# Optimization experiments

Measured on AMD Instinct MI355X. Metric: run time of the kernel, lower is better.

The kernel has to match this reference:

```python
import jax, jax.numpy as jnp
import numpy as np

D_MODEL, H, D_K, D_V = 512, 8, 64, 64
S_Q, S_KV = 2048, 2048


def setup_inputs() -> dict:
    key = jax.random.key(0)
    ks = jax.random.split(key, 11)
    sc = 0.02
    return {
        "embeddings": jax.random.normal(ks[0], (S_Q, D_MODEL), jnp.float32),
        "K": jax.random.normal(ks[1], (S_KV, D_MODEL), jnp.float32),
        "V": jax.random.normal(ks[2], (S_KV, D_MODEL), jnp.float32),
        # per-head projection weights (stacked over heads) + biases
        "Wq": jax.random.normal(ks[3], (H, D_MODEL, D_K), jnp.float32) * sc,
        "bq": jax.random.normal(ks[4], (H, D_K), jnp.float32) * sc,
        "Wk": jax.random.normal(ks[5], (H, D_MODEL, D_K), jnp.float32) * sc,
        "bk": jax.random.normal(ks[6], (H, D_K), jnp.float32) * sc,
        "Wv": jax.random.normal(ks[7], (H, D_MODEL, D_V), jnp.float32) * sc,
        "bv": jax.random.normal(ks[8], (H, D_V), jnp.float32) * sc,
        # final linear: [h*d_v -> d_model]
        "Wo": jax.random.normal(ks[9], (H * D_V, D_MODEL), jnp.float32) * sc,
        "bo": jax.random.normal(ks[10], (D_MODEL,), jnp.float32) * sc,
    }


def reference(embeddings, K, V, Wq, bq, Wk, bk, Wv, bv, Wo, bo):
    # Batched per-head projections (the original loops over h heads; math identical)
    q = jnp.einsum("sd,hdk->hsk", embeddings, Wq) + bq[:, None, :]  # [h, Sq, d_k]
    k = jnp.einsum("td,hdk->htk", K, Wk) + bk[:, None, :]           # [h, Skv, d_k]
    v = jnp.einsum("td,hdv->htv", V, Wv) + bv[:, None, :]           # [h, Skv, d_v]
    scores = jnp.einsum("hsk,htk->hst", q, k) / jnp.sqrt(jnp.asarray(D_K, q.dtype))
    attn = jax.nn.softmax(scores, axis=-1)                           # [h, Sq, Skv]
    out = jnp.einsum("hst,htv->hsv", attn, v)                        # [h, Sq, d_v]
    # torch.cat(results, dim=1): head 0's d_v columns first -> [Sq, h*d_v]
    concat = jnp.transpose(out, (1, 0, 2)).reshape(S_Q, H * D_V)
    return concat @ Wo + bo                                          # [Sq, d_model]
```

## Files before the change

### kernel.cpp

```cpp
#include <hip/hip_runtime.h>

#define SQ 2048
#define DM 512
#define NH 8
#define NSPLIT 4

typedef __bf16 bf16x8 __attribute__((ext_vector_type(8)));
typedef float f32x4 __attribute__((ext_vector_type(4)));
typedef unsigned short us8 __attribute__((ext_vector_type(8)));

__device__ __forceinline__ unsigned short f2bf(float f) {
    unsigned u = __builtin_bit_cast(unsigned, f);
    u += 0x7fffu + ((u >> 16) & 1u);
    return (unsigned short)(u >> 16);
}
__device__ __forceinline__ unsigned short f2bf_trunc(float f) {
    return (unsigned short)(__builtin_bit_cast(unsigned, f) >> 16);
}

__global__ __launch_bounds__(256) void convert_all(
    const float* __restrict__ emb, const float* __restrict__ Kin, const float* __restrict__ Vin,
    const float* __restrict__ Wq,  const float* __restrict__ Wk,  const float* __restrict__ Wv,
    const float* __restrict__ Wo,
    unsigned short* __restrict__ xe, unsigned short* __restrict__ xk, unsigned short* __restrict__ xv,
    unsigned short* __restrict__ Wt, unsigned short* __restrict__ Wot)
{
    const int b = blockIdx.x, tid = threadIdx.x;
    __shared__ float ld[64 * 68];
    float4* ld4 = reinterpret_cast<float4*>(ld);

    if (b < 1536) {
        const int m = b >> 9;
        const float* src = (m == 0) ? emb : (m == 1) ? Kin : Vin;
        unsigned short* dst = (m == 0) ? xe : (m == 1) ? xk : xv;
        const int oct = (b & 511) * 256 + tid;
        const float4* s4 = reinterpret_cast<const float4*>(src + (size_t)oct * 8);
        float4 f0 = s4[0], f1 = s4[1];
        us8 o;
        o[0] = f2bf(f0.x); o[1] = f2bf(f0.y); o[2] = f2bf(f0.z); o[3] = f2bf(f0.w);
        o[4] = f2bf(f1.x); o[5] = f2bf(f1.y); o[6] = f2bf(f1.z); o[7] = f2bf(f1.w);
        *reinterpret_cast<us8*>(dst + (size_t)oct * 8) = o;
    } else if (b < 1728) {
        const int wi = b - 1536;
        const int idx = wi >> 3;
        const int kt = wi & 7;
        const int p = idx >> 3, h = idx & 7;
        const float* src = ((p == 0) ? Wq : (p == 1) ? Wk : Wv)
                         + (size_t)h * 512 * 64 + (size_t)kt * 64 * 64;
        unsigned short* dst = Wt + (size_t)idx * 64 * 512 + kt * 64;
        const int rr = tid >> 4, c4 = tid & 15;
        #pragma unroll
        for (int it = 0; it < 4; it++) {
            int r = rr + 16 * it;
            ld4[r * 17 + c4] = reinterpret_cast<const float4*>(src + (size_t)r * 64)[c4];
        }
        __syncthreads();
        #pragma unroll
        for (int it = 0; it < 2; it++) {
            int slot = tid + it * 256;
            int n = slot >> 3, g = slot & 7;
            us8 o;
            #pragma unroll
            for (int i = 0; i < 8; i++)
                o[i] = f2bf(ld[(g * 8 + i) * 68 + n]);
            *reinterpret_cast<us8*>(dst + (size_t)n * 512 + g * 8) = o;
        }
    } else {
        const int ti = b - 1728;
        const int kt = ti >> 3, nt = ti & 7;
        const float* src = Wo + (size_t)kt * 64 * 512 + nt * 64;
        const int rr = tid >> 4, c4 = tid & 15;
        #pragma unroll
        for (int it = 0; it < 4; it++) {
            int r = rr + 16 * it;
            ld4[r * 17 + c4] = reinterpret_cast<const float4*>(src + (size_t)r * 512)[c4];
        }
        __syncthreads();
        #pragma unroll
        for (int it = 0; it < 2; it++) {
            int slot = tid + it * 256;
            int n = slot >> 3, g = slot & 7;
            us8 o;
            #pragma unroll
            for (int i = 0; i < 8; i++)
                o[i] = f2bf(ld[(g * 8 + i) * 68 + n]);
            *reinterpret_cast<us8*>(Wot + (size_t)(nt * 64 + n) * 512 + kt * 64 + g * 8) = o;
        }
    }
}

__global__ __launch_bounds__(256) void qkv_mfma(
    const unsigned short* __restrict__ xe, const unsigned short* __restrict__ xk,
    const unsigned short* __restrict__ xv, const unsigned short* __restrict__ Wt,
    const float* __restrict__ bq, const float* __restrict__ bk, const float* __restrict__ bv,
    unsigned short* __restrict__ qo, unsigned short* __restrict__ ko, unsigned short* __restrict__ vo)
{
    const int p = blockIdx.z, h = blockIdx.y, s0 = blockIdx.x * 64;
    const unsigned short* X = (p == 0) ? xe : (p == 1) ? xk : xv;
    const unsigned short* W = Wt + (size_t)(p * 8 + h) * 64 * 512;
    const float* B = ((p == 0) ? bq : (p == 1) ? bk : bv) + h * 64;

    const int tid = threadIdx.x;
    const int w = tid >> 6, lane = tid & 63, cl = lane & 15, q4 = lane >> 4;
    const int sr = tid >> 3, sg = tid & 7;

    __shared__ unsigned short As[2][64 * 72];
    __shared__ unsigned short Bs[2][64 * 72];

    #pragma unroll
    for (int it = 0; it < 2; it++) {
        int r = sr + 32 * it;
        *reinterpret_cast<float4*>(&As[0][r * 72 + sg * 8]) =
            *reinterpret_cast<const float4*>(&X[(size_t)(s0 + r) * 512 + sg * 8]);
        *reinterpret_cast<float4*>(&Bs[0][r * 72 + sg * 8]) =
            *reinterpret_cast<const float4*>(&W[(size_t)r * 512 + sg * 8]);
    }

    f32x4 acc[4] = {};

    for (int c = 0; c < 8; c++) {
        __syncthreads();
        const int buf = c & 1;
        const bool more = (c + 1 < 8);
        float4 ar[2], br[2];
        if (more) {
            #pragma unroll
            for (int it = 0; it < 2; it++) {
                int r = sr + 32 * it;
                ar[it] = *reinterpret_cast<const float4*>(
                    &X[(size_t)(s0 + r) * 512 + (c + 1) * 64 + sg * 8]);
                br[it] = *reinterpret_cast<const float4*>(
                    &W[(size_t)r * 512 + (c + 1) * 64 + sg * 8]);
            }
        }

        bf16x8 a0 = *reinterpret_cast<const bf16x8*>(&As[buf][(16 * w + cl) * 72 + q4 * 8]);
        bf16x8 a1 = *reinterpret_cast<const bf16x8*>(&As[buf][(16 * w + cl) * 72 + 32 + q4 * 8]);
        #pragma unroll
        for (int nn = 0; nn < 4; nn++) {
            bf16x8 b0 = *reinterpret_cast<const bf16x8*>(&Bs[buf][(16 * nn + cl) * 72 + q4 * 8]);
            bf16x8 b1 = *reinterpret_cast<const bf16x8*>(&Bs[buf][(16 * nn + cl) * 72 + 32 + q4 * 8]);
            acc[nn] = __builtin_amdgcn_mfma_f32_16x16x32_bf16(a0, b0, acc[nn], 0, 0, 0);
            acc[nn] = __builtin_amdgcn_mfma_f32_16x16x32_bf16(a1, b1, acc[nn], 0, 0, 0);
        }

        if (more) {
            const int nbuf = buf ^ 1;
            #pragma unroll
            for (int it = 0; it < 2; it++) {
                int r = sr + 32 * it;
                *reinterpret_cast<float4*>(&As[nbuf][r * 72 + sg * 8]) = ar[it];
                *reinterpret_cast<float4*>(&Bs[nbuf][r * 72 + sg * 8]) = br[it];
            }
        }
    }

    if (p == 0) {
        #pragma unroll
        for (int nn = 0; nn < 4; nn++) {
            int col = 16 * nn + cl;
            float bb = B[col];
            #pragma unroll
            for (int r = 0; r < 4; r++)
                qo[((size_t)h * SQ + s0 + 16 * w + q4 * 4 + r) * 64 + col] =
                    f2bf((acc[nn][r] + bb) * 0.125f);
        }
    } else if (p == 1) {
        #pragma unroll
        for (int nn = 0; nn < 4; nn++) {
            int col = 16 * nn + cl;
            float bb = B[col];
            #pragma unroll
            for (int r = 0; r < 4; r++)
                ko[((size_t)h * SQ + s0 + 16 * w + q4 * 4 + r) * 64 + col] =
                    f2bf(acc[nn][r] + bb);
        }
    } else {
        #pragma unroll
        for (int nn = 0; nn < 4; nn++) {
            int col = 16 * nn + cl;
            float bb = B[col];
            ushort4 o;
            o.x = f2bf(acc[nn][0] + bb);
            o.y = f2bf(acc[nn][1] + bb);
            o.z = f2bf(acc[nn][2] + bb);
            o.w = f2bf(acc[nn][3] + bb);
            *reinterpret_cast<ushort4*>(
                vo + ((size_t)h * 64 + col) * SQ + s0 + 16 * w + q4 * 4) = o;
        }
    }
}

#define PW 72

__global__ __launch_bounds__(256) void attn_fwd(
    const unsigned short* __restrict__ qbf,
    const unsigned short* __restrict__ kbf,
    const unsigned short* __restrict__ vbf,
    float* __restrict__ Opart,
    float* __restrict__ lpart)
{
    const int h = blockIdx.y, s0 = blockIdx.x * 64, z = blockIdx.z;
    const int tid = threadIdx.x;
    const int w = tid >> 6, lane = tid & 63, cl = lane & 15, q4 = lane >> 4;
    const int NT = SQ / 64 / NSPLIT;
    const int t0 = z * NT;

    __shared__ unsigned short Ks[2][64 * PW];
    __shared__ unsigned short Vs[2][64 * PW];
    __shared__ unsigned short Ps[4][16 * PW];

    bf16x8 aq0 = *reinterpret_cast<const bf16x8*>(
        &qbf[((size_t)h * SQ + s0 + 16 * w + cl) * 64 + q4 * 8]);
    bf16x8 aq1 = *reinterpret_cast<const bf16x8*>(
        &qbf[((size_t)h * SQ + s0 + 16 * w + cl) * 64 + 32 + q4 * 8]);

    const int sr = tid >> 3, sg = tid & 7;

    #pragma unroll
    for (int it = 0; it < 2; it++) {
        int r = sr + 32 * it;
        *reinterpret_cast<float4*>(&Ks[0][r * PW + sg * 8]) =
            *reinterpret_cast<const float4*>(&kbf[((size_t)h * SQ + t0 * 64 + r) * 64 + sg * 8]);
        *reinterpret_cast<float4*>(&Vs[0][r * PW + sg * 8]) =
            *reinterpret_cast<const float4*>(&vbf[((size_t)h * 64 + r) * SQ + t0 * 64 + sg * 8]);
    }

    f32x4 o_acc[4] = {};
    float lsum[4] = {};

    for (int tl = 0; tl < NT; tl++) {
        __syncthreads();
        const int buf = tl & 1;
        const bool more = (tl + 1 < NT);
        float4 kr[2], vr[2];
        if (more) {
            #pragma unroll
            for (int it = 0; it < 2; it++) {
                int r = sr + 32 * it;
                kr[it] = *reinterpret_cast<const float4*>(
                    &kbf[((size_t)h * SQ + (t0 + tl + 1) * 64 + r) * 64 + sg * 8]);
                vr[it] = *reinterpret_cast<const float4*>(
                    &vbf[((size_t)h * 64 + r) * SQ + (t0 + tl + 1) * 64 + sg * 8]);
            }
        }

        f32x4 s_acc[4] = {};
        #pragma unroll
        for (int nn = 0; nn < 4; nn++) {
            bf16x8 b0 = *reinterpret_cast<const bf16x8*>(&Ks[buf][(16 * nn + cl) * PW + q4 * 8]);
            bf16x8 b1 = *reinterpret_cast<const bf16x8*>(&Ks[buf][(16 * nn + cl) * PW + 32 + q4 * 8]);
            s_acc[nn] = __builtin_amdgcn_mfma_f32_16x16x32_bf16(aq0, b0, s_acc[nn], 0, 0, 0);
            s_acc[nn] = __builtin_amdgcn_mfma_f32_16x16x32_bf16(aq1, b1, s_acc[nn], 0, 0, 0);
        }

        #pragma unroll
        for (int r = 0; r < 4; r++) {
            #pragma unroll
            for (int nn = 0; nn < 4; nn++) {
                float pv = __expf(s_acc[nn][r]);
                lsum[r] += pv;
                Ps[w][(q4 * 4 + r) * PW + 16 * nn + cl] = f2bf_trunc(pv);
            }
        }
        bf16x8 ap0 = *reinterpret_cast<const bf16x8*>(&Ps[w][cl * PW + q4 * 8]);
        bf16x8 ap1 = *reinterpret_cast<const bf16x8*>(&Ps[w][cl * PW + 32 + q4 * 8]);

        #pragma unroll
        for (int nn = 0; nn < 4; nn++) {
            bf16x8 b0 = *reinterpret_cast<const bf16x8*>(&Vs[buf][(16 * nn + cl) * PW + q4 * 8]);
            bf16x8 b1 = *reinterpret_cast<const bf16x8*>(&Vs[buf][(16 * nn + cl) * PW + 32 + q4 * 8]);
            o_acc[nn] = __builtin_amdgcn_mfma_f32_16x16x32_bf16(ap0, b0, o_acc[nn], 0, 0, 0);
            o_acc[nn] = __builtin_amdgcn_mfma_f32_16x16x32_bf16(ap1, b1, o_acc[nn], 0, 0, 0);
        }

        if (more) {
            const int nbuf = buf ^ 1;
            #pragma unroll
            for (int it = 0; it < 2; it++) {
                int r = sr + 32 * it;
                *reinterpret_cast<float4*>(&Ks[nbuf][r * PW + sg * 8]) = kr[it];
                *reinterpret_cast<float4*>(&Vs[nbuf][r * PW + sg * 8]) = vr[it];
            }
        }
    }

    #pragma unroll
    for (int r = 0; r < 4; r++) {
        float v = lsum[r];
        #pragma unroll
        for (int off = 1; off < 16; off <<= 1) v += __shfl_xor(v, off);
        lsum[r] = v;
    }

    const size_t zb = (size_t)(z * NH + h);
    if (cl == 0) {
        #pragma unroll
        for (int r = 0; r < 4; r++)
            lpart[zb * SQ + s0 + 16 * w + q4 * 4 + r] = lsum[r];
    }
    #pragma unroll
    for (int nn = 0; nn < 4; nn++)
        #pragma unroll
        for (int r = 0; r < 4; r++)
            Opart[(zb * SQ + s0 + 16 * w + q4 * 4 + r) * 64 + 16 * nn + cl] = o_acc[nn][r];
}

__global__ __launch_bounds__(256) void out_proj(
    const float* __restrict__ Opart, const float* __restrict__ lpart,
    const unsigned short* __restrict__ Wot,
    const float* __restrict__ bo, float* __restrict__ out)
{
    const int s0 = blockIdx.x * 64, n0 = blockIdx.y * 64;
    const int tid = threadIdx.x;
    const int w = tid >> 6, lane = tid & 63, cl = lane & 15, q4 = lane >> 4;
    const int sr = tid >> 3, sg = tid & 7;

    __shared__ unsigned short As[2][64 * 72];
    __shared__ unsigned short Bs[2][64 * 72];
    __shared__ float invL[512];

    #pragma unroll
    for (int k = 0; k < 2; k++) {
        int idx = tid * 2 + k;
        int hh = idx >> 6, ss = idx & 63;
        float l = 0.f;
        #pragma unroll
        for (int z = 0; z < NSPLIT; z++)
            l += lpart[(size_t)(z * 8 + hh) * SQ + s0 + ss];
        invL[idx] = 1.0f / l;
    }
    __syncthreads();

    #pragma unroll
    for (int it = 0; it < 2; it++) {
        int r = sr + 32 * it;
        float o[8] = {};
        #pragma unroll
        for (int z = 0; z < NSPLIT; z++) {
            const float4* pp = reinterpret_cast<const float4*>(
                &Opart[((size_t)(z * 8) * SQ + s0 + r) * 64 + sg * 8]);
            float4 a = pp[0], b = pp[1];
            o[0] += a.x; o[1] += a.y; o[2] += a.z; o[3] += a.w;
            o[4] += b.x; o[5] += b.y; o[6] += b.z; o[7] += b.w;
        }
        float il = invL[r];
        us8 pk;
        #pragma unroll
        for (int i = 0; i < 8; i++) pk[i] = f2bf(o[i] * il);
        *reinterpret_cast<us8*>(&As[0][r * 72 + sg * 8]) = pk;
        *reinterpret_cast<float4*>(&Bs[0][r * 72 + sg * 8]) =
            *reinterpret_cast<const float4*>(&Wot[(size_t)(n0 + r) * 512 + sg * 8]);
    }

    f32x4 acc[4] = {};

    for (int c = 0; c < 8; c++) {
        __syncthreads();
        const int buf = c & 1;
        const bool more = (c + 1 < 8);
        float4 pre[2][NSPLIT][2];
        float4 wr[2];
        if (more) {
            const int hn = c + 1;
            #pragma unroll
            for (int it = 0; it < 2; it++) {
                int r = sr + 32 * it;
                #pragma unroll
                for (int z = 0; z < NSPLIT; z++) {
                    const float4* pp = reinterpret_cast<const float4*>(
                        &Opart[((size_t)(z * 8 + hn) * SQ + s0 + r) * 64 + sg * 8]);
                    pre[it][z][0] = pp[0];
                    pre[it][z][1] = pp[1];
                }
                wr[it] = *reinterpret_cast<const float4*>(
                    &Wot[(size_t)(n0 + r) * 512 + hn * 64 + sg * 8]);
            }
        }

        bf16x8 a0 = *reinterpret_cast<const bf16x8*>(&As[buf][(16 * w + cl) * 72 + q4 * 8]);
        bf16x8 a1 = *reinterpret_cast<const bf16x8*>(&As[buf][(16 * w + cl) * 72 + 32 + q4 * 8]);
        #pragma unroll
        for (int nn = 0; nn < 4; nn++) {
            bf16x8 b0 = *reinterpret_cast<const bf16x8*>(&Bs[buf][(16 * nn + cl) * 72 + q4 * 8]);
            bf16x8 b1 = *reinterpret_cast<const bf16x8*>(&Bs[buf][(16 * nn + cl) * 72 + 32 + q4 * 8]);
            acc[nn] = __builtin_amdgcn_mfma_f32_16x16x32_bf16(a0, b0, acc[nn], 0, 0, 0);
            acc[nn] = __builtin_amdgcn_mfma_f32_16x16x32_bf16(a1, b1, acc[nn], 0, 0, 0);
        }

        if (more) {
            const int nbuf = buf ^ 1;
            const int hn = c + 1;
            #pragma unroll
            for (int it = 0; it < 2; it++) {
                int r = sr + 32 * it;
                float o[8] = {};
                #pragma unroll
                for (int z = 0; z < NSPLIT; z++) {
                    float4 a = pre[it][z][0], b = pre[it][z][1];
                    o[0] += a.x; o[1] += a.y; o[2] += a.z; o[3] += a.w;
                    o[4] += b.x; o[5] += b.y; o[6] += b.z; o[7] += b.w;
                }
                float il = invL[hn * 64 + r];
                us8 pk;
                #pragma unroll
                for (int i = 0; i < 8; i++) pk[i] = f2bf(o[i] * il);
                *reinterpret_cast<us8*>(&As[nbuf][r * 72 + sg * 8]) = pk;
                *reinterpret_cast<float4*>(&Bs[nbuf][r * 72 + sg * 8]) = wr[it];
            }
        }
    }

    #pragma unroll
    for (int nn = 0; nn < 4; nn++) {
        int col = n0 + 16 * nn + cl;
        float bb = bo[col];
        #pragma unroll
        for (int r = 0; r < 4; r++)
            out[(size_t)(s0 + 16 * w + q4 * 4 + r) * DM + col] = acc[nn][r] + bb;
    }
}

extern "C" void kernel_launch(void* const* d_in, const int* in_sizes, int n_in,
                              void* d_out, int out_size, void* d_ws, size_t ws_size,
                              hipStream_t stream) {
    const float* emb = (const float*)d_in[0];
    const float* Kin = (const float*)d_in[1];
    const float* Vin = (const float*)d_in[2];
    const float* Wq  = (const float*)d_in[3];
    const float* bq  = (const float*)d_in[4];
    const float* Wk  = (const float*)d_in[5];
    const float* bk  = (const float*)d_in[6];
    const float* Wv  = (const float*)d_in[7];
    const float* bv  = (const float*)d_in[8];
    const float* Wo  = (const float*)d_in[9];
    const float* bo  = (const float*)d_in[10];
    float* out = (float*)d_out;

    unsigned short* p = (unsigned short*)d_ws;
    unsigned short* xe  = p; p += (size_t)SQ * DM;
    unsigned short* xk  = p; p += (size_t)SQ * DM;
    unsigned short* xv  = p; p += (size_t)SQ * DM;
    unsigned short* Wt  = p; p += (size_t)24 * 64 * 512;
    unsigned short* Wot = p; p += (size_t)512 * 512;
    unsigned short* qbf = p; p += (size_t)NH * SQ * 64;
    unsigned short* kbf = p; p += (size_t)NH * SQ * 64;
    unsigned short* vbf = p; p += (size_t)NH * SQ * 64;
    float* Opart = (float*)p;
    float* lpart = Opart + (size_t)NSPLIT * NH * SQ * 64;

    convert_all<<<1792, 256, 0, stream>>>(emb, Kin, Vin, Wq, Wk, Wv, Wo,
                                          xe, xk, xv, Wt, Wot);
    qkv_mfma<<<dim3(32, 8, 3), 256, 0, stream>>>(xe, xk, xv, Wt, bq, bk, bv,
                                                 qbf, kbf, vbf);
    attn_fwd<<<dim3(32, 8, NSPLIT), 256, 0, stream>>>(qbf, kbf, vbf, Opart, lpart);
    out_proj<<<dim3(32, 8), 256, 0, stream>>>(Opart, lpart, Wot, bo, out);
}
```

Before: 130.3 us.

## Split attention combine into separate kernel and single-buffer attn LDS tiles

Adds an attn_combine kernel that sums the split-KV partial outputs, normalizes them by the summed denominators and writes a bf16 concatenated attention tensor. out_proj then reads only that tensor, so each output-column block no longer re-reads all fp32 partials. In attn_fwd, the K/V shared-memory tiles go from double to single buffering, with register prefetch and an extra barrier per tile, to cut LDS use. This costs one more kernel launch and adds synchronization in the attention loop.

```diff
diff --git a/kernel.cpp b/kernel.cpp
--- a/kernel.cpp
+++ b/kernel.cpp
@@ -206,8 +206,8 @@
     const int NT = SQ / 64 / NSPLIT;
     const int t0 = z * NT;
 
-    __shared__ unsigned short Ks[2][64 * PW];
-    __shared__ unsigned short Vs[2][64 * PW];
+    __shared__ unsigned short Ks[64 * PW];
+    __shared__ unsigned short Vs[64 * PW];
     __shared__ unsigned short Ps[4][16 * PW];
 
     bf16x8 aq0 = *reinterpret_cast<const bf16x8*>(
@@ -217,24 +217,29 @@
 
     const int sr = tid >> 3, sg = tid & 7;
 
+    float4 kr[2], vr[2];
     #pragma unroll
     for (int it = 0; it < 2; it++) {
         int r = sr + 32 * it;
-        *reinterpret_cast<float4*>(&Ks[0][r * PW + sg * 8]) =
-            *reinterpret_cast<const float4*>(&kbf[((size_t)h * SQ + t0 * 64 + r) * 64 + sg * 8]);
-        *reinterpret_cast<float4*>(&Vs[0][r * PW + sg * 8]) =
-            *reinterpret_cast<const float4*>(&vbf[((size_t)h * 64 + r) * SQ + t0 * 64 + sg * 8]);
+        kr[it] = *reinterpret_cast<const float4*>(
+            &kbf[((size_t)h * SQ + t0 * 64 + r) * 64 + sg * 8]);
+        vr[it] = *reinterpret_cast<const float4*>(
+            &vbf[((size_t)h * 64 + r) * SQ + t0 * 64 + sg * 8]);
     }
 
     f32x4 o_acc[4] = {};
     float lsum[4] = {};
 
     for (int tl = 0; tl < NT; tl++) {
+        if (tl) __syncthreads();
+        #pragma unroll
+        for (int it = 0; it < 2; it++) {
+            int r = sr + 32 * it;
+            *reinterpret_cast<float4*>(&Ks[r * PW + sg * 8]) = kr[it];
+            *reinterpret_cast<float4*>(&Vs[r * PW + sg * 8]) = vr[it];
+        }
         __syncthreads();
-        const int buf = tl & 1;
-        const bool more = (tl + 1 < NT);
-        float4 kr[2], vr[2];
-        if (more) {
+        if (tl + 1 < NT) {
             #pragma unroll
             for (int it = 0; it < 2; it++) {
                 int r = sr + 32 * it;
@@ -248,8 +253,8 @@
         f32x4 s_acc[4] = {};
         #pragma unroll
         for (int nn = 0; nn < 4; nn++) {
-            bf16x8 b0 = *reinterpret_cast<const bf16x8*>(&Ks[buf][(16 * nn + cl) * PW + q4 * 8]);
-            bf16x8 b1 = *reinterpret_cast<const bf16x8*>(&Ks[buf][(16 * nn + cl) * PW + 32 + q4 * 8]);
+            bf16x8 b0 = *reinterpret_cast<const bf16x8*>(&Ks[(16 * nn + cl) * PW + q4 * 8]);
+            bf16x8 b1 = *reinterpret_cast<const bf16x8*>(&Ks[(16 * nn + cl) * PW + 32 + q4 * 8]);
             s_acc[nn] = __builtin_amdgcn_mfma_f32_16x16x32_bf16(aq0, b0, s_acc[nn], 0, 0, 0);
             s_acc[nn] = __builtin_amdgcn_mfma_f32_16x16x32_bf16(aq1, b1, s_acc[nn], 0, 0, 0);
         }
@@ -268,21 +273,11 @@
 
         #pragma unroll
         for (int nn = 0; nn < 4; nn++) {
-            bf16x8 b0 = *reinterpret_cast<const bf16x8*>(&Vs[buf][(16 * nn + cl) * PW + q4 * 8]);
-            bf16x8 b1 = *reinterpret_cast<const bf16x8*>(&Vs[buf][(16 * nn + cl) * PW + 32 + q4 * 8]);
+            bf16x8 b0 = *reinterpret_cast<const bf16x8*>(&Vs[(16 * nn + cl) * PW + q4 * 8]);
+            bf16x8 b1 = *reinterpret_cast<const bf16x8*>(&Vs[(16 * nn + cl) * PW + 32 + q4 * 8]);
             o_acc[nn] = __builtin_amdgcn_mfma_f32_16x16x32_bf16(ap0, b0, o_acc[nn], 0, 0, 0);
             o_acc[nn] = __builtin_amdgcn_mfma_f32_16x16x32_bf16(ap1, b1, o_acc[nn], 0, 0, 0);
         }
-
-        if (more) {
-            const int nbuf = buf ^ 1;
-            #pragma unroll
-            for (int it = 0; it < 2; it++) {
-                int r = sr + 32 * it;
-                *reinterpret_cast<float4*>(&Ks[nbuf][r * PW + sg * 8]) = kr[it];
-                *reinterpret_cast<float4*>(&Vs[nbuf][r * PW + sg * 8]) = vr[it];
-            }
-        }
     }
 
     #pragma unroll
@@ -306,9 +301,37 @@
             Opart[(zb * SQ + s0 + 16 * w + q4 * 4 + r) * 64 + 16 * nn + cl] = o_acc[nn][r];
 }
 
+__global__ __launch_bounds__(256) void attn_combine(
+    const float* __restrict__ Opart, const float* __restrict__ lpart,
+    unsigned short* __restrict__ att)
+{
+    const int gid = blockIdx.x * 256 + threadIdx.x;
+    const int s = gid >> 6, oct = gid & 63;
+    const int col0 = oct * 8, h = col0 >> 6, dv0 = col0 & 63;
+
+    float l = 0.f;
+    #pragma unroll
+    for (int z = 0; z < NSPLIT; z++)
+        l += lpart[(size_t)(z * NH + h) * SQ + s];
+    const float inv = 1.0f / l;
+
+    float o[8] = {};
+    #pragma unroll
+    for (int z = 0; z < NSPLIT; z++) {
+        const float4* base = reinterpret_cast<const float4*>(
+            Opart + ((size_t)(z * NH + h) * SQ + s) * 64 + dv0);
+        float4 a = base[0], b = base[1];
+        o[0] += a.x; o[1] += a.y; o[2] += a.z; o[3] += a.w;
+        o[4] += b.x; o[5] += b.y; o[6] += b.z; o[7] += b.w;
+    }
+    us8 pk;
+    #pragma unroll
+    for (int i = 0; i < 8; i++) pk[i] = f2bf(o[i] * inv);
+    *reinterpret_cast<us8*>(att + (size_t)s * DM + col0) = pk;
+}
+
 __global__ __launch_bounds__(256) void out_proj(
-    const float* __restrict__ Opart, const float* __restrict__ lpart,
-    const unsigned short* __restrict__ Wot,
+    const unsigned short* __restrict__ att, const unsigned short* __restrict__ Wot,
     const float* __restrict__ bo, float* __restrict__ out)
 {
     const int s0 = blockIdx.x * 64, n0 = blockIdx.y * 64;
@@ -318,37 +341,12 @@
 
     __shared__ unsigned short As[2][64 * 72];
     __shared__ unsigned short Bs[2][64 * 72];
-    __shared__ float invL[512];
-
-    #pragma unroll
-    for (int k = 0; k < 2; k++) {
-        int idx = tid * 2 + k;
-        int hh = idx >> 6, ss = idx & 63;
-        float l = 0.f;
-        #pragma unroll
-        for (int z = 0; z < NSPLIT; z++)
-            l += lpart[(size_t)(z * 8 + hh) * SQ + s0 + ss];
-        invL[idx] = 1.0f / l;
-    }
-    __syncthreads();
 
     #pragma unroll
     for (int it = 0; it < 2; it++) {
         int r = sr + 32 * it;
-        float o[8] = {};
-        #pragma unroll
-        for (int z = 0; z < NSPLIT; z++) {
-            const float4* pp = reinterpret_cast<const float4*>(
-                &Opart[((size_t)(z * 8) * SQ + s0 + r) * 64 + sg * 8]);
-            float4 a = pp[0], b = pp[1];
-            o[0] += a.x; o[1] += a.y; o[2] += a.z; o[3] += a.w;
-            o[4] += b.x; o[5] += b.y; o[6] += b.z; o[7] += b.w;
-        }
-        float il = invL[r];
-        us8 pk;
-        #pragma unroll
-        for (int i = 0; i < 8; i++) pk[i] = f2bf(o[i] * il);
-        *reinterpret_cast<us8*>(&As[0][r * 72 + sg * 8]) = pk;
+        *reinterpret_cast<float4*>(&As[0][r * 72 + sg * 8]) =
+            *reinterpret_cast<const float4*>(&att[(size_t)(s0 + r) * 512 + sg * 8]);
         *reinterpret_cast<float4*>(&Bs[0][r * 72 + sg * 8]) =
             *reinterpret_cast<const float4*>(&Wot[(size_t)(n0 + r) * 512 + sg * 8]);
     }
@@ -359,22 +357,15 @@
         __syncthreads();
         const int buf = c & 1;
         const bool more = (c + 1 < 8);
-        float4 pre[2][NSPLIT][2];
-        float4 wr[2];
+        float4 ar[2], br[2];
         if (more) {
-            const int hn = c + 1;
             #pragma unroll
             for (int it = 0; it < 2; it++) {
                 int r = sr + 32 * it;
-                #pragma unroll
-                for (int z = 0; z < NSPLIT; z++) {
-                    const float4* pp = reinterpret_cast<const float4*>(
-                        &Opart[((size_t)(z * 8 + hn) * SQ + s0 + r) * 64 + sg * 8]);
-                    pre[it][z][0] = pp[0];
-                    pre[it][z][1] = pp[1];
-                }
-                wr[it] = *reinterpret_cast<const float4*>(
-                    &Wot[(size_t)(n0 + r) * 512 + hn * 64 + sg * 8]);
+                ar[it] = *reinterpret_cast<const float4*>(
+                    &att[(size_t)(s0 + r) * 512 + (c + 1) * 64 + sg * 8]);
+                br[it] = *reinterpret_cast<const float4*>(
+                    &Wot[(size_t)(n0 + r) * 512 + (c + 1) * 64 + sg * 8]);
             }
         }
 
@@ -390,23 +381,11 @@
 
         if (more) {
             const int nbuf = buf ^ 1;
-            const int hn = c + 1;
             #pragma unroll
             for (int it = 0; it < 2; it++) {
                 int r = sr + 32 * it;
-                float o[8] = {};
-                #pragma unroll
-                for (int z = 0; z < NSPLIT; z++) {
-                    float4 a = pre[it][z][0], b = pre[it][z][1];
-                    o[0] += a.x; o[1] += a.y; o[2] += a.z; o[3] += a.w;
-                    o[4] += b.x; o[5] += b.y; o[6] += b.z; o[7] += b.w;
-                }
-                float il = invL[hn * 64 + r];
-                us8 pk;
-                #pragma unroll
-                for (int i = 0; i < 8; i++) pk[i] = f2bf(o[i] * il);
-                *reinterpret_cast<us8*>(&As[nbuf][r * 72 + sg * 8]) = pk;
-                *reinterpret_cast<float4*>(&Bs[nbuf][r * 72 + sg * 8]) = wr[it];
+                *reinterpret_cast<float4*>(&As[nbuf][r * 72 + sg * 8]) = ar[it];
+                *reinterpret_cast<float4*>(&Bs[nbuf][r * 72 + sg * 8]) = br[it];
             }
         }
     }
@@ -446,6 +425,7 @@
     unsigned short* qbf = p; p += (size_t)NH * SQ * 64;
     unsigned short* kbf = p; p += (size_t)NH * SQ * 64;
     unsigned short* vbf = p; p += (size_t)NH * SQ * 64;
+    unsigned short* att = p; p += (size_t)SQ * DM;
     float* Opart = (float*)p;
     float* lpart = Opart + (size_t)NSPLIT * NH * SQ * 64;
 
@@ -454,5 +434,6 @@
     qkv_mfma<<<dim3(32, 8, 3), 256, 0, stream>>>(xe, xk, xv, Wt, bq, bk, bv,
                                                  qbf, kbf, vbf);
     attn_fwd<<<dim3(32, 8, NSPLIT), 256, 0, stream>>>(qbf, kbf, vbf, Opart, lpart);
-    out_proj<<<dim3(32, 8), 256, 0, stream>>>(Opart, lpart, Wot, bo, out);
-}
+    attn_combine<<<512, 256, 0, stream>>>(Opart, lpart, att);
+    out_proj<<<dim3(32, 8), 256, 0, stream>>>(att, Wot, bo, out);
+}
```

After: 149.5 us. 1.15x slower.
